# Kernel optimization log

Measured on AMD Instinct MI355X. Metric: run time of the kernel, lower is better.

Reference implementation:

```python
import jax, jax.numpy as jnp
import numpy as np

TOP_K = 2


def setup_inputs() -> dict:
    key = jax.random.key(0)
    k1, k2 = jax.random.split(key)
    hidden_states = jax.random.normal(k1, (4, 4096, 4096), dtype=jnp.float32)
    gate_weight = jax.random.normal(k2, (8, 4096), dtype=jnp.float32) * 0.02
    return {"hidden_states": hidden_states, "gate_weight": gate_weight}


def reference(hidden_states, gate_weight):
    # router logits: [B, S, E]
    router_logits = jnp.einsum("bsh,eh->bse", hidden_states, gate_weight)
    routing_weights = jax.nn.softmax(router_logits, axis=-1)
    # top-k over experts, then renormalize
    topk_weights, selected_experts = jax.lax.top_k(routing_weights, TOP_K)
    topk_weights = topk_weights / jnp.sum(topk_weights, axis=-1, keepdims=True)
    return (topk_weights, selected_experts)
```

## Files before the change

### kernel.cpp

```cpp
#include <hip/hip_runtime.h>
#include <math.h>


#define HDIM 4096
#define NEXP 8
#define KCHUNK 1024
#define NCHUNK (HDIM / KCHUNK)
#define TOK_PER_WAVE 4
#define WAVES_PER_BLOCK 4
#define TOK_PER_BLOCK (TOK_PER_WAVE * WAVES_PER_BLOCK)

__global__ __launch_bounds__(256, 4) void moe_gate_kernel(
    const float* __restrict__ hidden,
    const float* __restrict__ gate_w,
    float* __restrict__ out,
    int n_tokens) {
  __shared__ float wlds[NEXP * KCHUNK];

  const int tid  = threadIdx.x;
  const int wave = tid >> 6;
  const int lane = tid & 63;
  const int tbase = blockIdx.x * TOK_PER_BLOCK + wave * TOK_PER_WAVE;

  float acc[TOK_PER_WAVE][NEXP];
#pragma unroll
  for (int t = 0; t < TOK_PER_WAVE; ++t)
#pragma unroll
    for (int e = 0; e < NEXP; ++e) acc[t][e] = 0.f;

  for (int c = 0; c < NCHUNK; ++c) {
    __syncthreads();
#pragma unroll
    for (int j = 0; j < 8; ++j) {
      const int fid = j * 256 + tid;
      const int e   = fid >> 8;
      const int k4  = fid & 255;
      const float4 v = *(const float4*)(gate_w + (size_t)e * HDIM + c * KCHUNK + k4 * 4);
      *(float4*)(wlds + e * KCHUNK + k4 * 4) = v;
    }
    __syncthreads();

    const int kbase = c * KCHUNK;
#pragma unroll
    for (int s = 0; s < KCHUNK / 256; ++s) {
      const int kloc = (s * 64 + lane) * 4;
      float4 h4[TOK_PER_WAVE];
#pragma unroll
      for (int t = 0; t < TOK_PER_WAVE; ++t)
        h4[t] = *(const float4*)(hidden + (size_t)(tbase + t) * HDIM + kbase + kloc);
#pragma unroll
      for (int e = 0; e < NEXP; ++e) {
        const float4 w4 = *(const float4*)(wlds + e * KCHUNK + kloc);
#pragma unroll
        for (int t = 0; t < TOK_PER_WAVE; ++t) {
          acc[t][e] += h4[t].x * w4.x;
          acc[t][e] += h4[t].y * w4.y;
          acc[t][e] += h4[t].z * w4.z;
          acc[t][e] += h4[t].w * w4.w;
        }
      }
    }
  }

#pragma unroll
  for (int t = 0; t < TOK_PER_WAVE; ++t) {
#pragma unroll
    for (int e = 0; e < NEXP; ++e) {
      float v = acc[t][e];
#pragma unroll
      for (int m = 1; m < 64; m <<= 1) v += __shfl_xor(v, m, 64);
      acc[t][e] = v;
    }
  }

  if (lane < TOK_PER_WAVE) {
    const int token = tbase + lane;
    if (token < n_tokens) {
      float l[NEXP];
#pragma unroll
      for (int e = 0; e < NEXP; ++e) {
        float v = acc[0][e];
        if (lane == 1) v = acc[1][e];
        if (lane == 2) v = acc[2][e];
        if (lane == 3) v = acc[3][e];
        l[e] = v;
      }
      int i1 = 0; float v1 = l[0];
#pragma unroll
      for (int e = 1; e < NEXP; ++e)
        if (l[e] > v1) { v1 = l[e]; i1 = e; }
      int i2 = (i1 == 0) ? 1 : 0; float v2 = l[(i1 == 0) ? 1 : 0];
#pragma unroll
      for (int e = 0; e < NEXP; ++e)
        if (e != i1 && l[e] > v2) { v2 = l[e]; i2 = e; }

      const float w1 = 1.0f / (1.0f + expf(v2 - v1));
      const float w2 = 1.0f - w1;

      const int nw = 2 * n_tokens;
      out[token * 2 + 0] = w1;
      out[token * 2 + 1] = w2;
      out[nw + token * 2 + 0] = (float)i1;
      out[nw + token * 2 + 1] = (float)i2;
    }
  }
}

extern "C" void kernel_launch(void* const* d_in, const int* in_sizes, int n_in,
                              void* d_out, int out_size, void* d_ws, size_t ws_size,
                              hipStream_t stream) {
  const float* hidden = (const float*)d_in[0];
  const float* gate_w = (const float*)d_in[1];
  float* out = (float*)d_out;

  const int n_tokens = in_sizes[0] / HDIM;
  const int grid = (n_tokens + TOK_PER_BLOCK - 1) / TOK_PER_BLOCK;
  moe_gate_kernel<<<grid, 256, 0, stream>>>(hidden, gate_w, out, n_tokens);
}
```

Before: 367.3 us.

## Drop LDS staging of gate weights, read from cache, nontemporal hidden loads

Removes the shared-memory staging of gate weights and the block-wide barriers, so each wave reads the 128KB gate matrix directly from global memory (expected to hit L2/L1) while streaming hidden states with nontemporal loads. Tokens per wave drop from 4 to 2, which doubles the grid and lowers register pressure at the cost of more weight traffic per token. An early exit for waves past the end is added. The kernel is bandwidth-bound on 256MB of hidden data, so the gain depends on whether weight reads stay cached and do not compete with the streaming loads.

```diff
diff --git a/kernel.cpp b/kernel.cpp
--- a/kernel.cpp
+++ b/kernel.cpp
@@ -4,23 +4,23 @@
 
 #define HDIM 4096
 #define NEXP 8
-#define KCHUNK 1024
-#define NCHUNK (HDIM / KCHUNK)
-#define TOK_PER_WAVE 4
+#define TOK_PER_WAVE 2
 #define WAVES_PER_BLOCK 4
 #define TOK_PER_BLOCK (TOK_PER_WAVE * WAVES_PER_BLOCK)
+#define KSTEPS (HDIM / (64 * 4))
+
+typedef float f32x4 __attribute__((ext_vector_type(4)));
 
 __global__ __launch_bounds__(256, 4) void moe_gate_kernel(
     const float* __restrict__ hidden,
     const float* __restrict__ gate_w,
     float* __restrict__ out,
     int n_tokens) {
-  __shared__ float wlds[NEXP * KCHUNK];
-
   const int tid  = threadIdx.x;
   const int wave = tid >> 6;
   const int lane = tid & 63;
   const int tbase = blockIdx.x * TOK_PER_BLOCK + wave * TOK_PER_WAVE;
+  if (tbase >= n_tokens) return;
 
   float acc[TOK_PER_WAVE][NEXP];
 #pragma unroll
@@ -28,37 +28,25 @@
 #pragma unroll
     for (int e = 0; e < NEXP; ++e) acc[t][e] = 0.f;
 
-  for (int c = 0; c < NCHUNK; ++c) {
-    __syncthreads();
+  const float* h0 = hidden + (size_t)tbase * HDIM;
+  const float* h1 = h0 + HDIM;
+
+#pragma unroll 2
+  for (int it = 0; it < KSTEPS; ++it) {
+    const int koff = (it * 64 + lane) * 4;
+    const f32x4 ha = __builtin_nontemporal_load((const f32x4*)(h0 + koff));
+    const f32x4 hb = __builtin_nontemporal_load((const f32x4*)(h1 + koff));
 #pragma unroll
-    for (int j = 0; j < 8; ++j) {
-      const int fid = j * 256 + tid;
-      const int e   = fid >> 8;
-      const int k4  = fid & 255;
-      const float4 v = *(const float4*)(gate_w + (size_t)e * HDIM + c * KCHUNK + k4 * 4);
-      *(float4*)(wlds + e * KCHUNK + k4 * 4) = v;
-    }
-    __syncthreads();
-
-    const int kbase = c * KCHUNK;
-#pragma unroll
-    for (int s = 0; s < KCHUNK / 256; ++s) {
-      const int kloc = (s * 64 + lane) * 4;
-      float4 h4[TOK_PER_WAVE];
-#pragma unroll
-      for (int t = 0; t < TOK_PER_WAVE; ++t)
-        h4[t] = *(const float4*)(hidden + (size_t)(tbase + t) * HDIM + kbase + kloc);
-#pragma unroll
-      for (int e = 0; e < NEXP; ++e) {
-        const float4 w4 = *(const float4*)(wlds + e * KCHUNK + kloc);
-#pragma unroll
-        for (int t = 0; t < TOK_PER_WAVE; ++t) {
-          acc[t][e] += h4[t].x * w4.x;
-          acc[t][e] += h4[t].y * w4.y;
-          acc[t][e] += h4[t].z * w4.z;
-          acc[t][e] += h4[t].w * w4.w;
-        }
-      }
+    for (int e = 0; e < NEXP; ++e) {
+      const f32x4 w4 = *(const f32x4*)(gate_w + e * HDIM + koff);
+      acc[0][e] += ha.x * w4.x;
+      acc[0][e] += ha.y * w4.y;
+      acc[0][e] += ha.z * w4.z;
+      acc[0][e] += ha.w * w4.w;
+      acc[1][e] += hb.x * w4.x;
+      acc[1][e] += hb.y * w4.y;
+      acc[1][e] += hb.z * w4.z;
+      acc[1][e] += hb.w * w4.w;
     }
   }
 
@@ -81,8 +69,6 @@
       for (int e = 0; e < NEXP; ++e) {
         float v = acc[0][e];
         if (lane == 1) v = acc[1][e];
-        if (lane == 2) v = acc[2][e];
-        if (lane == 3) v = acc[3][e];
         l[e] = v;
       }
       int i1 = 0; float v1 = l[0];
```

Result: no change. 362.0 us, median of 2 (-1.5%).
